# Kernel optimization log

Hardware: AMD Instinct MI355X
Metric: run time of the kernel (lower is better)

## Reference

```python
import jax, jax.numpy as jnp
import numpy as np
import math

B, N, NODE_DIM, STATE_DIM, EMB = 256, 2048, 3, 4, 128
NORM = 1.0 / math.sqrt(EMB)

def _uniform(key, shape, fan):
    stdv = 1.0 / math.sqrt(fan)
    return jax.random.uniform(key, shape, jnp.float32, -stdv, stdv)

def setup_inputs() -> dict:
    key = jax.random.key(0)
    ks = jax.random.split(key, 16)
    node_feats = jax.random.normal(ks[0], (B, N, NODE_DIM), jnp.float32)
    state = jax.random.normal(ks[1], (B, STATE_DIM), jnp.float32)
    curr_node_id = jax.random.randint(ks[2], (B,), 0, N)
    next_node_id = jax.random.randint(ks[3], (B,), 0, N)
    mask = jax.random.randint(ks[4], (B, N), 0, 2).astype(bool)
    return {
        'node_feats': node_feats,
        'state': state,
        'W_node': _uniform(ks[5], (NODE_DIM, EMB), EMB),
        'b_node': _uniform(ks[6], (EMB,), EMB),
        'W_depot': _uniform(ks[7], (2, EMB), EMB),
        'b_depot': _uniform(ks[8], (EMB,), EMB),
        'W_state': _uniform(ks[9], (STATE_DIM, EMB), EMB),
        'b_state': _uniform(ks[10], (EMB,), EMB),
        'w_q': _uniform(ks[11], (3 * EMB, EMB), EMB),
        'w_k': _uniform(ks[12], (2 * EMB, EMB), EMB),
        'w_v': _uniform(ks[13], (2 * EMB, EMB), EMB),
        'curr_node_id': curr_node_id,
        'next_node_id': next_node_id,
        'mask': mask,
    }

def reference(node_feats, state, W_node, b_node, W_depot, b_depot, W_state, b_state, w_q, w_k, w_v, curr_node_id, next_node_id, mask):
    # embed non-depot nodes and depot (first 2 coords only)
    node_emb = node_feats[:, 1:, :] @ W_node + b_node            # [B, N-1, E]
    depot_emb = node_feats[:, 0:1, :2] @ W_depot + b_depot      # [B, 1, E]
    nf = jnp.concatenate([depot_emb, node_emb], axis=1)          # [B, N, E]  (dropout=0 -> identity)
    curr_emb = jnp.take_along_axis(nf, curr_node_id[:, None, None], axis=1)  # [B, 1, E]
    next_emb = jnp.take_along_axis(nf, next_node_id[:, None, None], axis=1)  # [B, 1, E]
    state_emb = state @ W_state + b_state                        # [B, E]
    input_q = jnp.concatenate([curr_emb, next_emb, state_emb[:, None, :]], axis=-1)  # [B, 1, 3E]
    input_kv = jnp.concatenate([jnp.broadcast_to(curr_emb, nf.shape), nf], axis=-1)  # [B, N, 2E]
    q = input_q @ w_q                                            # [B, 1, E]
    k = input_kv @ w_k                                           # [B, N, E]
    v = input_kv @ w_v                                           # [B, N, E]
    compat = NORM * jnp.einsum('bqe,bne->bqn', q, k)             # [B, 1, N]
    compat = jnp.where(mask[:, None, :], compat, -jnp.inf)
    attn = jax.nn.softmax(compat, axis=-1)
    h = jnp.einsum('bqn,bne->bqe', attn, v)[:, 0, :]             # [B, E]
    return h
```

## Files before the change

kernel.cpp:

```cpp
#include <hip/hip_runtime.h>
#include <math.h>

#define NB 256
#define NN 2048
#define NE 128
#define NORMC 0.08838834764831845f


__device__ __constant__ int c_lid[47] = {
  0,1,2,3, 4,5,6,
  0,1,2,3, 4,5,6,
  7,8,9,10,11,
  0,1,2,3, 4,5,6,
  0,1,2,3, 4,5,6,
  0,1,2,3, 4,5,6,
  0,1,2,3, 4,5,6
};
__device__ __constant__ int c_rid[47] = {
  0,0,0,0,0,0,0,
  1,1,1,1,1,1,1,
  2,2,2,2,2,
  3,3,3,3,3,3,3,
  4,4,4,4,4,4,4,
  5,5,5,5,5,5,5,
  6,6,6,6,6,6,6
};

__global__ __launch_bounds__(128)
void k1_tables(const float* __restrict__ Wn, const float* __restrict__ bn,
               const float* __restrict__ Wd, const float* __restrict__ bd,
               const float* __restrict__ Ws, const float* __restrict__ bs,
               const float* __restrict__ wq, const float* __restrict__ wk,
               const float* __restrict__ wv, const void* __restrict__ maskp,
               float* __restrict__ T)
{
  const int r = blockIdx.x, e = threadIdx.x;
  if (r == 47) {
    __shared__ int sflag;
    if (e == 0) sflag = 0;
    __syncthreads();
    const unsigned char* mb = (const unsigned char*)maskp;
    int f = 0;
    #pragma unroll
    for (int i = 0; i < 32; ++i) {
      int idx = e * 32 + i;
      unsigned char v = mb[idx];
      if (v) { if (idx & 3) f |= 1; else if (idx & 7) f |= 2; }
    }
    if (f) atomicOr(&sflag, f);
    __syncthreads();
    if (e == 0) ((int*)T)[47 * NE] = sflag;
    return;
  }
  const int li = c_lid[r], ri = c_rid[r];
  const float* lv =
    (li < 3)  ? Wn + li * NE :
    (li == 3) ? bn :
    (li < 6)  ? Wd + (li - 4) * NE :
    (li == 6) ? bd :
    (li < 11) ? Ws + (li - 7) * NE : bs;
  const float* rv =
    (ri == 0) ? wq :
    (ri == 1) ? wq + 128 * NE :
    (ri == 2) ? wq + 256 * NE :
    (ri == 3) ? wk :
    (ri == 4) ? wk + 128 * NE :
    (ri == 5) ? wv : wv + 128 * NE;
  float acc = 0.f;
  #pragma unroll 32
  for (int j = 0; j < 128; ++j) acc += lv[j] * rv[j * NE + e];
  T[r * NE + e] = acc;
}

__global__ __launch_bounds__(1024)
void k2_main(const float* __restrict__ nodef,
             const float* __restrict__ state,
             const int*   __restrict__ curr_id,
             const int*   __restrict__ next_id,
             const void*  __restrict__ maskp,
             const float* __restrict__ T,
             float* __restrict__ out)
{
  const int b = blockIdx.x, t = threadIdx.x;

  __shared__ float qv[NE], kcs[NE];
  __shared__ float scal[8];
  __shared__ float redm[16], redsum[64];
  __shared__ float sse0;

  const int mflag = ((const int*)T)[47 * NE];
  const int cid = curr_id[b], nid = next_id[b];
  const float* xcp = nodef + ((size_t)b * NN + cid) * 3;
  const float* xnp = nodef + ((size_t)b * NN + nid) * 3;
  const float xc0 = xcp[0], xc1 = xcp[1], xc2 = xcp[2];
  const float xn0 = xnp[0], xn1 = xnp[1], xn2 = xnp[2];
  const float st0 = state[b*4], st1 = state[b*4+1], st2 = state[b*4+2], st3 = state[b*4+3];
  const float nf00 = nodef[(size_t)b * NN * 3];
  const float nf01 = nodef[(size_t)b * NN * 3 + 1];

  const float2* f2 = (const float2*)(nodef + (size_t)b * NN * 3);
  const float2 p0 = f2[3*t], p1 = f2[3*t+1], p2 = f2[3*t+2];

  long long mk0, mk1;
  {
    const size_t off = (size_t)b * NN + 2*t;
    if (mflag & 1)      { const unsigned char* m = (const unsigned char*)maskp; mk0 = m[off]; mk1 = m[off+1]; }
    else if (mflag & 2) { const int* m = (const int*)maskp;                     mk0 = m[off]; mk1 = m[off+1]; }
    else                { const long long* m = (const long long*)maskp;         mk0 = m[off]; mk1 = m[off+1]; }
  }

  float tg0 = 0.f, tg1 = 0.f;
  {
    const int gg = t >> 6, l = t & 63;
    if (t < 512 && gg >= 1) {
      const float* vg = (gg == 1) ? T + 29*NE :
                        (gg == 2) ? T + 32*NE :
                        (gg <= 5) ? T + (23 + gg)*NE :
                                    T + (24 + gg)*NE;
      tg0 = vg[l]; tg1 = vg[64 + l];
    }
  }

  float vc_r = 0.f, eav0=0.f, eav1=0.f, eav2=0.f, ecv=0.f, edv0=0.f, edv1=0.f, edv=0.f;
  if (t < NE) {
    const int e = t;
    float q, kc;
    if (cid == 0) {
      q  = xc0*T[ 4*NE+e] + xc1*T[ 5*NE+e] + T[ 6*NE+e];
      kc = xc0*T[23*NE+e] + xc1*T[24*NE+e] + T[25*NE+e];
      vc_r = xc0*T[37*NE+e] + xc1*T[38*NE+e] + T[39*NE+e];
    } else {
      q  = xc0*T[ 0*NE+e] + xc1*T[ 1*NE+e] + xc2*T[ 2*NE+e] + T[ 3*NE+e];
      kc = xc0*T[19*NE+e] + xc1*T[20*NE+e] + xc2*T[21*NE+e] + T[22*NE+e];
      vc_r = xc0*T[33*NE+e] + xc1*T[34*NE+e] + xc2*T[35*NE+e] + T[36*NE+e];
    }
    if (nid == 0) q += xn0*T[11*NE+e] + xn1*T[12*NE+e] + T[13*NE+e];
    else          q += xn0*T[ 7*NE+e] + xn1*T[ 8*NE+e] + xn2*T[ 9*NE+e] + T[10*NE+e];
    q += st0*T[14*NE+e] + st1*T[15*NE+e] + st2*T[16*NE+e] + st3*T[17*NE+e] + T[18*NE+e];
    qv[e] = q; kcs[e] = kc;
    eav0 = T[40*NE+e]; eav1 = T[41*NE+e]; eav2 = T[42*NE+e]; ecv = T[43*NE+e];
    edv0 = T[44*NE+e]; edv1 = T[45*NE+e]; edv  = T[46*NE+e];
  }
  __syncthreads();

  if (t < 512) {
    const int gg = t >> 6, l = t & 63;
    if (gg == 0) { tg0 = kcs[l]; tg1 = kcs[64 + l]; }
    float p = qv[l] * tg0 + qv[64 + l] * tg1;
    #pragma unroll
    for (int o = 32; o; o >>= 1) p += __shfl_down(p, o, 64);
    if (l == 0) scal[gg] = p;
  }
  __syncthreads();

  const float qkc = scal[0], qck = scal[1], qdk = scal[2];
  const float gk0 = scal[3], gk1 = scal[4], gk2 = scal[5];
  const float gdk0 = scal[6], gdk1 = scal[7];

  float c0, c1;
  if (t == 0) c0 = qkc + qdk + p0.x*gdk0 + p0.y*gdk1;
  else        c0 = qkc + qck + p0.x*gk0 + p0.y*gk1 + p1.x*gk2;
  c1 = qkc + qck + p1.y*gk0 + p2.x*gk1 + p2.y*gk2;
  c0 = mk0 ? c0 * NORMC : -INFINITY;
  c1 = mk1 ? c1 * NORMC : -INFINITY;

  float lmax = fmaxf(c0, c1);
  #pragma unroll
  for (int o = 32; o; o >>= 1) lmax = fmaxf(lmax, __shfl_down(lmax, o, 64));
  if ((t & 63) == 0) redm[t >> 6] = lmax;
  __syncthreads();
  float m = redm[0];
  #pragma unroll
  for (int i = 1; i < 16; ++i) m = fmaxf(m, redm[i]);

  const float ex0 = __expf(c0 - m);
  const float ex1 = __expf(c1 - m);
  if (t == 0) sse0 = ex0;
  float le = ex0 + ex1;
  float s0, s1, s2;
  if (t == 0) { s0 = ex1*p1.y; s1 = ex1*p2.x; s2 = ex1*p2.y; }
  else {
    s0 = ex0*p0.x + ex1*p1.y;
    s1 = ex0*p0.y + ex1*p2.x;
    s2 = ex0*p1.x + ex1*p2.y;
  }
  #pragma unroll
  for (int o = 32; o; o >>= 1) {
    le += __shfl_down(le, o, 64);
    s0 += __shfl_down(s0, o, 64);
    s1 += __shfl_down(s1, o, 64);
    s2 += __shfl_down(s2, o, 64);
  }
  if ((t & 63) == 0) {
    const int w = t >> 6;
    redsum[w] = le; redsum[16+w] = s0; redsum[32+w] = s1; redsum[48+w] = s2;
  }
  __syncthreads();

  if (t < NE) {
    float L = 0, S0 = 0, S1 = 0, S2 = 0;
    #pragma unroll
    for (int i = 0; i < 16; ++i) {
      L += redsum[i]; S0 += redsum[16+i]; S1 += redsum[32+i]; S2 += redsum[48+i];
    }
    const float a0 = sse0 / L;
    const float hv = vc_r
      + (1.0f - a0) * ecv
      + (S0*eav0 + S1*eav1 + S2*eav2) / L
      + a0 * (nf00*edv0 + nf01*edv1 + edv);
    out[(size_t)b * NE + t] = hv;
  }
}

extern "C" void kernel_launch(void* const* d_in, const int* in_sizes, int n_in,
                              void* d_out, int out_size, void* d_ws, size_t ws_size,
                              hipStream_t stream) {
  (void)in_sizes; (void)n_in; (void)out_size; (void)ws_size;
  const float* nodef   = (const float*)d_in[0];
  const float* state   = (const float*)d_in[1];
  const float* W_node  = (const float*)d_in[2];
  const float* b_node  = (const float*)d_in[3];
  const float* W_depot = (const float*)d_in[4];
  const float* b_depot = (const float*)d_in[5];
  const float* W_state = (const float*)d_in[6];
  const float* b_state = (const float*)d_in[7];
  const float* w_q     = (const float*)d_in[8];
  const float* w_k     = (const float*)d_in[9];
  const float* w_v     = (const float*)d_in[10];
  const int*   curr_id = (const int*)d_in[11];
  const int*   next_id = (const int*)d_in[12];
  const void*  maskp   = d_in[13];
  float* T   = (float*)d_ws;
  float* out = (float*)d_out;

  hipLaunchKernelGGL(k1_tables, dim3(48), dim3(128), 0, stream,
                     W_node, b_node, W_depot, b_depot, W_state, b_state,
                     w_q, w_k, w_v, maskp, T);
  hipLaunchKernelGGL(k2_main, dim3(NB), dim3(1024), 0, stream,
                     nodef, state, curr_id, next_id, maskp, T, out);
}
```

Before: 15.10 us.

## Stage weight tables in LDS, prefetch inputs into cache, widen per-thread work

The table kernel now uses 7 large blocks that stage each 128x128 weight slice and the small left-hand vectors in shared memory before forming the projected rows. Another 249 blocks stream node_feats and mask through the cache hierarchy so the main kernel finds them warm. The mask dtype flag is now detected inside the main kernel with wave ballots, replacing the separate detection block. Each main-kernel block uses 512 threads handling 4 nodes each, and every wave computes q redundantly so one barrier and the LDS staging disappear. The risks are that the prefetch adds a full extra pass over the inputs to the first kernel, and that the redundant q computation adds per-wave work.

```diff
diff --git a/kernel.cpp b/kernel.cpp
--- a/kernel.cpp
+++ b/kernel.cpp
@@ -7,72 +7,70 @@
 #define NORMC 0.08838834764831845f
 
 
-__device__ __constant__ int c_lid[47] = {
-  0,1,2,3, 4,5,6,
-  0,1,2,3, 4,5,6,
-  7,8,9,10,11,
-  0,1,2,3, 4,5,6,
-  0,1,2,3, 4,5,6,
-  0,1,2,3, 4,5,6,
-  0,1,2,3, 4,5,6
-};
-__device__ __constant__ int c_rid[47] = {
-  0,0,0,0,0,0,0,
-  1,1,1,1,1,1,1,
-  2,2,2,2,2,
-  3,3,3,3,3,3,3,
-  4,4,4,4,4,4,4,
-  5,5,5,5,5,5,5,
-  6,6,6,6,6,6,6
-};
-
-__global__ __launch_bounds__(128)
+__global__ __launch_bounds__(1024)
 void k1_tables(const float* __restrict__ Wn, const float* __restrict__ bn,
                const float* __restrict__ Wd, const float* __restrict__ bd,
                const float* __restrict__ Ws, const float* __restrict__ bs,
                const float* __restrict__ wq, const float* __restrict__ wk,
-               const float* __restrict__ wv, const void* __restrict__ maskp,
-               float* __restrict__ T)
+               const float* __restrict__ wv, const float* __restrict__ nodef,
+               const void* __restrict__ maskp, float* __restrict__ T)
 {
-  const int r = blockIdx.x, e = threadIdx.x;
-  if (r == 47) {
-    __shared__ int sflag;
-    if (e == 0) sflag = 0;
+  const int b = blockIdx.x, t = threadIdx.x;
+  if (b < 7) {
+    __shared__ float sW[128 * 128];
+    __shared__ float sLv[7 * 128];
+    const float* mat; int rowbase;
+    switch (b) {
+      case 0: mat = wq;          rowbase = 0;  break;
+      case 1: mat = wq + 16384;  rowbase = 7;  break;
+      case 2: mat = wq + 32768;  rowbase = 14; break;
+      case 3: mat = wk;          rowbase = 19; break;
+      case 4: mat = wk + 16384;  rowbase = 26; break;
+      case 5: mat = wv;          rowbase = 33; break;
+      default: mat = wv + 16384; rowbase = 40; break;
+    }
+    const int nrows = (b == 2) ? 5 : 7;
+    {
+      const float4* s4 = (const float4*)mat;
+      float4* d4 = (float4*)sW;
+      #pragma unroll
+      for (int i = 0; i < 4; ++i) d4[t + i * 1024] = s4[t + i * 1024];
+    }
+    if (b == 2) {
+      if (t < 512)      sLv[t] = Ws[t];
+      else if (t < 640) sLv[t] = bs[t - 512];
+    } else {
+      if (t < 384)      sLv[t] = Wn[t];
+      else if (t < 512) sLv[t] = bn[t - 384];
+      else if (t < 768) sLv[t] = Wd[t - 512];
+      else if (t < 896) sLv[t] = bd[t - 768];
+    }
     __syncthreads();
-    const unsigned char* mb = (const unsigned char*)maskp;
-    int f = 0;
-    #pragma unroll
-    for (int i = 0; i < 32; ++i) {
-      int idx = e * 32 + i;
-      unsigned char v = mb[idx];
-      if (v) { if (idx & 3) f |= 1; else if (idx & 7) f |= 2; }
-    }
-    if (f) atomicOr(&sflag, f);
-    __syncthreads();
-    if (e == 0) ((int*)T)[47 * NE] = sflag;
-    return;
-  }
-  const int li = c_lid[r], ri = c_rid[r];
-  const float* lv =
-    (li < 3)  ? Wn + li * NE :
-    (li == 3) ? bn :
-    (li < 6)  ? Wd + (li - 4) * NE :
-    (li == 6) ? bd :
-    (li < 11) ? Ws + (li - 7) * NE : bs;
-  const float* rv =
-    (ri == 0) ? wq :
-    (ri == 1) ? wq + 128 * NE :
-    (ri == 2) ? wq + 256 * NE :
-    (ri == 3) ? wk :
-    (ri == 4) ? wk + 128 * NE :
-    (ri == 5) ? wv : wv + 128 * NE;
-  float acc = 0.f;
-  #pragma unroll 32
-  for (int j = 0; j < 128; ++j) acc += lv[j] * rv[j * NE + e];
-  T[r * NE + e] = acc;
+    const int r = t >> 7, e = t & 127;
+    if (r < nrows) {
+      float acc = 0.f;
+      #pragma unroll 16
+      for (int j = 0; j < 128; ++j) acc += sLv[r * 128 + j] * sW[j * 128 + e];
+      T[(rowbase + r) * NE + e] = acc;
+    }
+  } else {
+    const float4* nf4 = (const float4*)nodef;
+    float fs = 0.f;
+    for (int i = (b - 7) * 1024 + t; i < NB * NN * 3 / 4; i += 249 * 1024) {
+      float4 v = nf4[i];
+      fs += v.x + v.y + v.z + v.w;
+    }
+    const uint4* mu = (const uint4*)maskp;
+    unsigned int ms = 0;
+    for (int i = (b - 7) * 1024 + t; i < 32768; i += 249 * 1024) {
+      uint4 v = mu[i];
+      ms |= v.x | v.y | v.z | v.w;
+    }
+    asm volatile("" :: "v"(fs), "v"(ms));
+  }
 }
 
-__global__ __launch_bounds__(1024)
+__global__ __launch_bounds__(512)
 void k2_main(const float* __restrict__ nodef,
              const float* __restrict__ state,
              const int*   __restrict__ curr_id,
@@ -82,74 +80,101 @@
              float* __restrict__ out)
 {
   const int b = blockIdx.x, t = threadIdx.x;
-
-  __shared__ float qv[NE], kcs[NE];
+  const int w = t >> 6, l = t & 63;
+
   __shared__ float scal[8];
-  __shared__ float redm[16], redsum[64];
+  __shared__ float redm[8], redsum[4][8];
   __shared__ float sse0;
 
-  const int mflag = ((const int*)T)[47 * NE];
+  const float4* A4 = (const float4*)(nodef + (size_t)b * (NN * 3));
+  const float4 a0 = A4[3 * t], a1 = A4[3 * t + 1], a2 = A4[3 * t + 2];
+
   const int cid = curr_id[b], nid = next_id[b];
+  const float4 st4 = *(const float4*)(state + b * 4);
   const float* xcp = nodef + ((size_t)b * NN + cid) * 3;
   const float* xnp = nodef + ((size_t)b * NN + nid) * 3;
   const float xc0 = xcp[0], xc1 = xcp[1], xc2 = xcp[2];
   const float xn0 = xnp[0], xn1 = xnp[1], xn2 = xnp[2];
-  const float st0 = state[b*4], st1 = state[b*4+1], st2 = state[b*4+2], st3 = state[b*4+3];
   const float nf00 = nodef[(size_t)b * NN * 3];
   const float nf01 = nodef[(size_t)b * NN * 3 + 1];
 
-  const float2* f2 = (const float2*)(nodef + (size_t)b * NN * 3);
-  const float2 p0 = f2[3*t], p1 = f2[3*t+1], p2 = f2[3*t+2];
-
-  long long mk0, mk1;
+  int mflag;
   {
-    const size_t off = (size_t)b * NN + 2*t;
-    if (mflag & 1)      { const unsigned char* m = (const unsigned char*)maskp; mk0 = m[off]; mk1 = m[off+1]; }
-    else if (mflag & 2) { const int* m = (const int*)maskp;                     mk0 = m[off]; mk1 = m[off+1]; }
-    else                { const long long* m = (const long long*)maskp;         mk0 = m[off]; mk1 = m[off+1]; }
-  }
-
-  float tg0 = 0.f, tg1 = 0.f;
+    const longlong2 mv = ((const longlong2*)maskp)[t];
+    const unsigned int w0 = (unsigned int)mv.x, w1 = (unsigned int)((unsigned long long)mv.x >> 32);
+    const unsigned int w2 = (unsigned int)mv.y, w3 = (unsigned int)((unsigned long long)mv.y >> 32);
+    int f = 0;
+    if ((w0 | w1 | w2 | w3) & 0xFFFFFF00u) f |= 1;
+    if ((w1 & 0xFFu) | (w3 & 0xFFu))       f |= 2;
+    const unsigned long long B1 = __ballot(f & 1);
+    const unsigned long long B2 = __ballot(f & 2);
+    mflag = B1 ? 1 : (B2 ? 2 : 4);
+  }
+
+  int mk0, mk1, mk2, mk3;
   {
-    const int gg = t >> 6, l = t & 63;
-    if (t < 512 && gg >= 1) {
-      const float* vg = (gg == 1) ? T + 29*NE :
-                        (gg == 2) ? T + 32*NE :
-                        (gg <= 5) ? T + (23 + gg)*NE :
-                                    T + (24 + gg)*NE;
-      tg0 = vg[l]; tg1 = vg[64 + l];
-    }
-  }
-
-  float vc_r = 0.f, eav0=0.f, eav1=0.f, eav2=0.f, ecv=0.f, edv0=0.f, edv1=0.f, edv=0.f;
+    const size_t off = (size_t)b * NN + 4 * (size_t)t;
+    if (mflag == 1) {
+      const unsigned int mm = *(const unsigned int*)((const unsigned char*)maskp + off);
+      mk0 = mm & 0xFF; mk1 = (mm >> 8) & 0xFF; mk2 = (mm >> 16) & 0xFF; mk3 = (mm >> 24) & 0xFF;
+    } else if (mflag == 2) {
+      const int4 mm = *(const int4*)((const int*)maskp + off);
+      mk0 = mm.x; mk1 = mm.y; mk2 = mm.z; mk3 = mm.w;
+    } else {
+      const longlong2* mp = (const longlong2*)maskp;
+      const longlong2 u = mp[off / 2], v = mp[off / 2 + 1];
+      mk0 = u.x != 0; mk1 = u.y != 0; mk2 = v.x != 0; mk3 = v.y != 0;
+    }
+  }
+
+  float evc = 0.f, eav0 = 0.f, eav1 = 0.f, eav2 = 0.f, ecv = 0.f, edv0 = 0.f, edv1 = 0.f, edv = 0.f;
   if (t < NE) {
     const int e = t;
-    float q, kc;
-    if (cid == 0) {
-      q  = xc0*T[ 4*NE+e] + xc1*T[ 5*NE+e] + T[ 6*NE+e];
-      kc = xc0*T[23*NE+e] + xc1*T[24*NE+e] + T[25*NE+e];
-      vc_r = xc0*T[37*NE+e] + xc1*T[38*NE+e] + T[39*NE+e];
-    } else {
-      q  = xc0*T[ 0*NE+e] + xc1*T[ 1*NE+e] + xc2*T[ 2*NE+e] + T[ 3*NE+e];
-      kc = xc0*T[19*NE+e] + xc1*T[20*NE+e] + xc2*T[21*NE+e] + T[22*NE+e];
-      vc_r = xc0*T[33*NE+e] + xc1*T[34*NE+e] + xc2*T[35*NE+e] + T[36*NE+e];
-    }
-    if (nid == 0) q += xn0*T[11*NE+e] + xn1*T[12*NE+e] + T[13*NE+e];
-    else          q += xn0*T[ 7*NE+e] + xn1*T[ 8*NE+e] + xn2*T[ 9*NE+e] + T[10*NE+e];
-    q += st0*T[14*NE+e] + st1*T[15*NE+e] + st2*T[16*NE+e] + st3*T[17*NE+e] + T[18*NE+e];
-    qv[e] = q; kcs[e] = kc;
+    const float vn0 = T[33*NE+e], vn1 = T[34*NE+e], vn2 = T[35*NE+e], vn3 = T[36*NE+e];
+    const float vd0 = T[37*NE+e], vd1 = T[38*NE+e], vd2 = T[39*NE+e];
+    evc = (cid == 0) ? (xc0*vd0 + xc1*vd1 + vd2)
+                     : (xc0*vn0 + xc1*vn1 + xc2*vn2 + vn3);
     eav0 = T[40*NE+e]; eav1 = T[41*NE+e]; eav2 = T[42*NE+e]; ecv = T[43*NE+e];
     edv0 = T[44*NE+e]; edv1 = T[45*NE+e]; edv  = T[46*NE+e];
   }
-  __syncthreads();
-
-  if (t < 512) {
-    const int gg = t >> 6, l = t & 63;
-    if (gg == 0) { tg0 = kcs[l]; tg1 = kcs[64 + l]; }
-    float p = qv[l] * tg0 + qv[64 + l] * tg1;
+
+  float qh[2];
+  #pragma unroll
+  for (int h = 0; h < 2; ++h) {
+    const int e = l + 64 * h;
+    const float cn0 = T[0*NE+e], cn1 = T[1*NE+e], cn2 = T[2*NE+e], cn3 = T[3*NE+e];
+    const float cd0 = T[4*NE+e], cd1 = T[5*NE+e], cd2 = T[6*NE+e];
+    const float nn0 = T[7*NE+e], nn1 = T[8*NE+e], nn2 = T[9*NE+e], nn3 = T[10*NE+e];
+    const float nd0 = T[11*NE+e], nd1 = T[12*NE+e], nd2 = T[13*NE+e];
+    const float s0 = T[14*NE+e], s1 = T[15*NE+e], s2 = T[16*NE+e], s3 = T[17*NE+e], s4 = T[18*NE+e];
+    float q = (cid == 0) ? (xc0*cd0 + xc1*cd1 + cd2)
+                         : (xc0*cn0 + xc1*cn1 + xc2*cn2 + cn3);
+    q += (nid == 0) ? (xn0*nd0 + xn1*nd1 + nd2)
+                    : (xn0*nn0 + xn1*nn1 + xn2*nn2 + nn3);
+    q += st4.x*s0 + st4.y*s1 + st4.z*s2 + st4.w*s3 + s4;
+    qh[h] = q;
+  }
+
+  {
+    float tgl, tgh;
+    if (w == 0) {
+      #pragma unroll
+      for (int h = 0; h < 2; ++h) {
+        const int e = l + 64 * h;
+        const float kn0 = T[19*NE+e], kn1 = T[20*NE+e], kn2 = T[21*NE+e], kn3 = T[22*NE+e];
+        const float kd0 = T[23*NE+e], kd1 = T[24*NE+e], kd2 = T[25*NE+e];
+        const float kc = (cid == 0) ? (xc0*kd0 + xc1*kd1 + kd2)
+                                    : (xc0*kn0 + xc1*kn1 + xc2*kn2 + kn3);
+        if (h == 0) tgl = kc; else tgh = kc;
+      }
+    } else {
+      const int row = (w == 1) ? 29 : (w == 2) ? 32 : (w <= 5) ? (23 + w) : (24 + w);
+      tgl = T[row*NE + l]; tgh = T[row*NE + 64 + l];
+    }
+    float p = qh[0] * tgl + qh[1] * tgh;
     #pragma unroll
     for (int o = 32; o; o >>= 1) p += __shfl_down(p, o, 64);
-    if (l == 0) scal[gg] = p;
+    if (l == 0) scal[w] = p;
   }
   __syncthreads();
 
@@ -157,33 +182,39 @@
   const float gk0 = scal[3], gk1 = scal[4], gk2 = scal[5];
   const float gdk0 = scal[6], gdk1 = scal[7];
 
-  float c0, c1;
-  if (t == 0) c0 = qkc + qdk + p0.x*gdk0 + p0.y*gdk1;
-  else        c0 = qkc + qck + p0.x*gk0 + p0.y*gk1 + p1.x*gk2;
-  c1 = qkc + qck + p1.y*gk0 + p2.x*gk1 + p2.y*gk2;
+  const float f0 = a0.x, f1 = a0.y, f2 = a0.z, f3 = a0.w;
+  const float f4 = a1.x, f5 = a1.y, f6 = a1.z, f7 = a1.w;
+  const float f8 = a2.x, f9 = a2.y, f10 = a2.z, f11 = a2.w;
+  float c0, c1, c2, c3;
+  if (t == 0) c0 = qkc + qdk + f0*gdk0 + f1*gdk1;
+  else        c0 = qkc + qck + f0*gk0 + f1*gk1 + f2*gk2;
+  c1 = qkc + qck + f3*gk0 + f4*gk1 + f5*gk2;
+  c2 = qkc + qck + f6*gk0 + f7*gk1 + f8*gk2;
+  c3 = qkc + qck + f9*gk0 + f10*gk1 + f11*gk2;
   c0 = mk0 ? c0 * NORMC : -INFINITY;
   c1 = mk1 ? c1 * NORMC : -INFINITY;
-
-  float lmax = fmaxf(c0, c1);
+  c2 = mk2 ? c2 * NORMC : -INFINITY;
+  c3 = mk3 ? c3 * NORMC : -INFINITY;
+
+  float lmax = fmaxf(fmaxf(c0, c1), fmaxf(c2, c3));
   #pragma unroll
   for (int o = 32; o; o >>= 1) lmax = fmaxf(lmax, __shfl_down(lmax, o, 64));
-  if ((t & 63) == 0) redm[t >> 6] = lmax;
+  if (l == 0) redm[w] = lmax;
   __syncthreads();
   float m = redm[0];
   #pragma unroll
-  for (int i = 1; i < 16; ++i) m = fmaxf(m, redm[i]);
-
-  const float ex0 = __expf(c0 - m);
-  const float ex1 = __expf(c1 - m);
-  if (t == 0) sse0 = ex0;
-  float le = ex0 + ex1;
+  for (int i = 1; i < 8; ++i) m = fmaxf(m, redm[i]);
+
+  const float e0 = __expf(c0 - m), e1 = __expf(c1 - m);
+  const float e2 = __expf(c2 - m), e3 = __expf(c3 - m);
+  if (t == 0) sse0 = e0;
+  float le = e0 + e1 + e2 + e3;
   float s0, s1, s2;
-  if (t == 0) { s0 = ex1*p1.y; s1 = ex1*p2.x; s2 = ex1*p2.y; }
-  else {
-    s0 = ex0*p0.x + ex1*p1.y;
-    s1 = ex0*p0.y + ex1*p2.x;
-    s2 = ex0*p1.x + ex1*p2.y;
-  }
+  if (t == 0) { s0 = 0.f; s1 = 0.f; s2 = 0.f; }
+  else        { s0 = e0*f0; s1 = e0*f1; s2 = e0*f2; }
+  s0 += e1*f3 + e2*f6 + e3*f9;
+  s1 += e1*f4 + e2*f7 + e3*f10;
+  s2 += e1*f5 + e2*f8 + e3*f11;
   #pragma unroll
   for (int o = 32; o; o >>= 1) {
     le += __shfl_down(le, o, 64);
@@ -191,23 +222,20 @@
     s1 += __shfl_down(s1, o, 64);
     s2 += __shfl_down(s2, o, 64);
   }
-  if ((t & 63) == 0) {
-    const int w = t >> 6;
-    redsum[w] = le; redsum[16+w] = s0; redsum[32+w] = s1; redsum[48+w] = s2;
-  }
+  if (l == 0) { redsum[0][w] = le; redsum[1][w] = s0; redsum[2][w] = s1; redsum[3][w] = s2; }
   __syncthreads();
 
   if (t < NE) {
-    float L = 0, S0 = 0, S1 = 0, S2 = 0;
+    float L = 0.f, S0 = 0.f, S1 = 0.f, S2 = 0.f;
     #pragma unroll
-    for (int i = 0; i < 16; ++i) {
-      L += redsum[i]; S0 += redsum[16+i]; S1 += redsum[32+i]; S2 += redsum[48+i];
-    }
-    const float a0 = sse0 / L;
-    const float hv = vc_r
-      + (1.0f - a0) * ecv
+    for (int i = 0; i < 8; ++i) {
+      L += redsum[0][i]; S0 += redsum[1][i]; S1 += redsum[2][i]; S2 += redsum[3][i];
+    }
+    const float a0w = sse0 / L;
+    const float hv = evc
+      + (1.0f - a0w) * ecv
       + (S0*eav0 + S1*eav1 + S2*eav2) / L
-      + a0 * (nf00*edv0 + nf01*edv1 + edv);
+      + a0w * (nf00*edv0 + nf01*edv1 + edv);
     out[(size_t)b * NE + t] = hv;
   }
 }
@@ -233,9 +261,9 @@
   float* T   = (float*)d_ws;
   float* out = (float*)d_out;
 
-  hipLaunchKernelGGL(k1_tables, dim3(48), dim3(128), 0, stream,
+  hipLaunchKernelGGL(k1_tables, dim3(256), dim3(1024), 0, stream,
                      W_node, b_node, W_depot, b_depot, W_state, b_state,
-                     w_q, w_k, w_v, maskp, T);
-  hipLaunchKernelGGL(k2_main, dim3(NB), dim3(1024), 0, stream,
+                     w_q, w_k, w_v, nodef, maskp, T);
+  hipLaunchKernelGGL(k2_main, dim3(NB), dim3(512), 0, stream,
                      nodef, state, curr_id, next_id, maskp, T, out);
 }
```

Result: no change. 15.34 us (+1.6%).
